# Performance work log

Measured on AMD Instinct MI355X. Metric: run time of the kernel, lower is better.

Reference implementation:

```python
import jax, jax.numpy as jnp
import numpy as np

B, N, D = 2, 2048, 512
H, VD = 8, 64  # v_dim = hid_dim / n_head


def setup_inputs() -> dict:
    key = jax.random.key(0)
    k1, k2, k3, k4 = jax.random.split(key, 4)
    inputs = jax.random.normal(k1, (B, N, D), dtype=jnp.float32)
    # lecun_normal: std = 1/sqrt(fan_in) with fan_in = D
    s = 1.0 / np.sqrt(D)
    q_w = jax.random.normal(k2, (H, D, VD), dtype=jnp.float32) * s
    k_w = jax.random.normal(k3, (H, D, VD), dtype=jnp.float32) * s
    v_w = jax.random.normal(k4, (H, D, VD), dtype=jnp.float32) * s
    return {"inputs": inputs, "q_w": q_w, "k_w": k_w, "v_w": v_w}


def reference(inputs, q_w, k_w, v_w):
    # QKV projections: [B,N,D] x [H,D,VD] -> [B,H,N,VD]
    q = jnp.einsum('bnj,hjk->bhnk', inputs, q_w)
    k = jnp.einsum('bnj,hjk->bhnk', inputs, k_w)
    v = jnp.einsum('bnj,hjk->bhnk', inputs, v_w)
    scale = 1.0 / jnp.sqrt(jnp.asarray(VD, dtype=q.dtype))
    scores = jnp.einsum('bhik,bhjk->bhij', q, k) * scale  # [B,H,N,N]
    att = jax.nn.softmax(scores, axis=-1)
    out = jnp.einsum('bhnj,bhjd->bhnd', att, v)  # [B,H,N,VD]
    out = jnp.transpose(out, (0, 2, 1, 3)).reshape(inputs.shape[0], -1, H * VD)  # [B,N,hid_dim]
    # keras GELU default is exact (non-approximate)
    return jax.nn.gelu(out, approximate=False)
```

## Files before the change

kernel.cpp:

```cpp
#include <hip/hip_runtime.h>
#include <hip/hip_bf16.h>
#include <math.h>

#define BB 2
#define NN 2048
#define DD 512
#define HH 8
#define VD 64

typedef _Float16 half8 __attribute__((ext_vector_type(8)));
typedef _Float16 half4 __attribute__((ext_vector_type(4)));
typedef __fp16 fp16x2 __attribute__((ext_vector_type(2)));
typedef float f32x4 __attribute__((ext_vector_type(4)));

#define GLDS16(gp, lp) __builtin_amdgcn_global_load_lds( \
    (const __attribute__((address_space(1))) void*)(gp), \
    (__attribute__((address_space(3))) void*)(lp), 16, 0, 0)

__device__ __forceinline__ float fexp2(float x) {
#if __has_builtin(__builtin_amdgcn_exp2f)
    return __builtin_amdgcn_exp2f(x);
#else
    return exp2f(x);
#endif
}

__device__ __forceinline__ void stage8(const _Float16* gsrc, size_t ldg, int r0,
                                       _Float16* lbase, int lane) {
    int r8 = lane >> 3;
    int ce = ((lane & 7) ^ r8) << 3;
    const _Float16* g = gsrc + (size_t)(r0 + r8) * ldg + ce;
    GLDS16(g, lbase);
}

__device__ __forceinline__ half8 frag_ld(const _Float16* tile, int row, int cb) {
    int off = row * 128 + (cb ^ ((row & 7) << 4));
    return *(const half8*)((const char*)tile + off);
}

__device__ __forceinline__ half8 frag_ldv(const _Float16* tile, int row, int cb) {
    int off = row * 256 + (cb ^ ((row & 15) << 4));
    return *(const half8*)((const char*)tile + off);
}

__device__ __forceinline__ float gelu_exact(float v) {
    return 0.5f * v * (1.f + erff(v * 0.70710678118654752f));
}

__global__ __launch_bounds__(256) void prep_kernel(
    const float* __restrict__ x,
    const float* __restrict__ qw, const float* __restrict__ kw,
    const float* __restrict__ vw,
    _Float16* __restrict__ wt, _Float16* __restrict__ xh)
{
    __shared__ float ls[64][65];
    const int t = threadIdx.x;
    const int bid = blockIdx.x;
    if (bid < 192) {
        const int kc = bid & 7, h = (bid >> 3) & 7, ty = bid >> 6;
        const float* src = (ty == 0) ? qw : (ty == 1) ? kw : vw;
#pragma unroll
        for (int j = 0; j < 4; ++j) {
            int idx = t + 256 * j;
            int k = idx >> 4, o4 = idx & 15;
            float4 v = *(const float4*)(src + ((size_t)(h * DD + kc * 64 + k) * VD + o4 * 4));
            ls[k][o4 * 4 + 0] = v.x; ls[k][o4 * 4 + 1] = v.y;
            ls[k][o4 * 4 + 2] = v.z; ls[k][o4 * 4 + 3] = v.w;
        }
        __syncthreads();
#pragma unroll
        for (int j = 0; j < 4; ++j) {
            int idx = t + 256 * j;
            int o = idx >> 4, k4 = idx & 15;
            half4 hv;
#pragma unroll
            for (int i = 0; i < 4; ++i) hv[i] = (_Float16)ls[k4 * 4 + i][o];
            *(half4*)(wt + ((size_t)(ty * HH + h) * VD + o) * DD + kc * 64 + k4 * 4) = hv;
        }
    } else {
        size_t idx = ((size_t)(bid - 192) * 256 + t) * 8;
        float4 a = *(const float4*)(x + idx);
        float4 b = *(const float4*)(x + idx + 4);
        half8 hv;
        hv[0] = (_Float16)a.x; hv[1] = (_Float16)a.y;
        hv[2] = (_Float16)a.z; hv[3] = (_Float16)a.w;
        hv[4] = (_Float16)b.x; hv[5] = (_Float16)b.y;
        hv[6] = (_Float16)b.z; hv[7] = (_Float16)b.w;
        *(half8*)(xh + idx) = hv;
    }
}

__global__ __launch_bounds__(256, 1) void qkv_proj_kernel(
    const _Float16* __restrict__ xh,
    const _Float16* __restrict__ wt,
    _Float16* __restrict__ qsp,
    _Float16* __restrict__ kbp,
    _Float16* __restrict__ vtp)
{
    __shared__ __align__(16) _Float16 xls[2][8192];
    __shared__ __align__(16) _Float16 wls[2][12288];
    const int t = threadIdx.x;
    const int wave = t >> 6, lane = t & 63;
    const int lq = lane & 15, g = lane >> 4;
    const int bid = blockIdx.x;
    const int h = bid & 7;
    const int m0 = (bid >> 3) * 128;
    const int rbase = 64 * (wave >> 1);
    const int cbase = 96 * (wave & 1);

    f32x4 acc[4][6];
#pragma unroll
    for (int a = 0; a < 4; ++a)
#pragma unroll
        for (int c = 0; c < 6; ++c) acc[a][c] = (f32x4){0.f, 0.f, 0.f, 0.f};

    auto stage = [&](int buf, int ks) {
#pragma unroll
        for (int j = 0; j < 4; ++j) {
            int i = wave * 4 + j;
            stage8(xh + (size_t)m0 * DD + ks * 64, DD, i * 8, &xls[buf][i * 512], lane);
        }
#pragma unroll
        for (int j = 0; j < 6; ++j) {
            int i = wave * 6 + j;
            int ty = i >> 3;
            int ol = (i & 7) * 8;
            stage8(wt + ((size_t)(ty * HH + h) * VD + ol) * DD + ks * 64, DD, 0,
                   &wls[buf][i * 512], lane);
        }
    };

    stage(0, 0);
    stage(1, 1);
    for (int ks = 0; ks < 8; ++ks) {
        const int buf = ks & 1;
        if (ks < 7) asm volatile("s_waitcnt vmcnt(10)" ::: "memory");
        else        asm volatile("s_waitcnt vmcnt(0)" ::: "memory");
        __builtin_amdgcn_s_barrier();
        half8 af[4][2];
        half8 bf[6][2];
#pragma unroll
        for (int amt = 0; amt < 4; ++amt) {
            af[amt][0] = frag_ld(xls[buf], rbase + amt * 16 + lq, 16 * g);
            af[amt][1] = frag_ld(xls[buf], rbase + amt * 16 + lq, 64 + 16 * g);
        }
#pragma unroll
        for (int ct = 0; ct < 6; ++ct) {
            int wr = cbase + ct * 16 + lq;
            bf[ct][0] = frag_ld(wls[buf], wr, 16 * g);
            bf[ct][1] = frag_ld(wls[buf], wr, 64 + 16 * g);
        }
        asm volatile("s_waitcnt lgkmcnt(0)" ::: "memory");
        __builtin_amdgcn_sched_barrier(0);
        __builtin_amdgcn_s_barrier();
        if (ks + 2 < 8) stage(buf, ks + 2);
        __builtin_amdgcn_s_setprio(1);
#pragma unroll
        for (int ct = 0; ct < 6; ++ct) {
#pragma unroll
            for (int amt = 0; amt < 4; ++amt) {
                acc[amt][ct] = __builtin_amdgcn_mfma_f32_16x16x32_f16(af[amt][0], bf[ct][0], acc[amt][ct], 0, 0, 0);
                acc[amt][ct] = __builtin_amdgcn_mfma_f32_16x16x32_f16(af[amt][1], bf[ct][1], acc[amt][ct], 0, 0, 0);
            }
        }
        __builtin_amdgcn_s_setprio(0);
    }

#pragma unroll
    for (int ct = 0; ct < 6; ++ct) {
        int gcol = cbase + ct * 16 + lq;
        int ty = gcol >> 6, o = gcol & 63;
#pragma unroll
        for (int amt = 0; amt < 4; ++amt) {
#pragma unroll
            for (int i = 0; i < 4; ++i) {
                int ng = m0 + rbase + amt * 16 + 4 * g + i;
                int b = ng >> 11, nb = ng & (NN - 1);
                size_t bh = (size_t)(b * HH + h);
                float v = acc[amt][ct][i];
                if (ty == 0)      qsp[(bh * NN + nb) * VD + o] = (_Float16)(v * 0.18033688011112042f);
                else if (ty == 1) kbp[(bh * NN + nb) * VD + o] = (_Float16)v;
                else {
                    int nbp = (nb & ~31) | (((nb >> 2) & 3) << 3) | (((nb >> 4) & 1) << 2) | (nb & 3);
                    vtp[(bh * VD + o) * NN + nbp] = (_Float16)v;
                }
            }
        }
    }
}

__global__ __launch_bounds__(256, 2) void attn_kernel(
    const _Float16* __restrict__ qs,
    const _Float16* __restrict__ kb,
    const _Float16* __restrict__ vt,
    float* __restrict__ out)
{
    constexpr int NITER = NN / 128;
    __shared__ __align__(16) char SM[65536 + 1024];
    const int t = threadIdx.x;
    const int wave = t >> 6, lane = t & 63;
    const int lq = lane & 15, g = lane >> 4;
    const int bid = blockIdx.x;
    const int xcd = bid & 7;
    const int bh = xcd * 2 + ((bid >> 3) & 1);
    const int qt = bid >> 4;
    const int qbase = qt * 64;

    half8 qf[4][2];
#pragma unroll
    for (int qg = 0; qg < 4; ++qg)
#pragma unroll
        for (int ds = 0; ds < 2; ++ds)
            qf[qg][ds] = *(const half8*)(qs + ((size_t)bh * NN + qbase + 16 * qg + lq) * VD + 32 * ds + 8 * g);

    const int r8 = lane >> 3;
    const _Float16* kS = kb + ((size_t)bh * NN + 32 * wave + r8) * VD + 8 * ((lane & 7) ^ r8);
    const _Float16* vS[4];
#pragma unroll
    for (int uu = 0; uu < 4; ++uu) {
        int vrow = 16 * wave + 4 * uu + g;
        vS[uu] = vt + ((size_t)bh * VD + vrow) * NN + 8 * (lq ^ (vrow & 15));
    }

    _Float16* kb0 = (_Float16*)(SM);
    _Float16* vb0 = (_Float16*)(SM + 16384);
    _Float16* kb1 = (_Float16*)(SM + 32768);
    _Float16* vb1 = (_Float16*)(SM + 49152);

    auto stage = [&](int b, int j) {
        _Float16* kd = (b ? kb1 : kb0) + 4 * wave * 512;
        const _Float16* kp = kS + (size_t)j * 128 * VD;
#pragma unroll
        for (int uu = 0; uu < 4; ++uu)
            GLDS16(kp + uu * 8 * VD, kd + uu * 512);
        _Float16* vd = (b ? vb1 : vb0) + 4 * wave * 512;
#pragma unroll
        for (int uu = 0; uu < 4; ++uu)
            GLDS16(vS[uu] + j * 128, vd + uu * 512);
    };

    f32x4 oacc[4][4];
    f32x4 oacc_l[4];
#pragma unroll
    for (int qg = 0; qg < 4; ++qg) {
#pragma unroll
        for (int dt = 0; dt < 4; ++dt) oacc[qg][dt] = (f32x4){0.f, 0.f, 0.f, 0.f};
        oacc_l[qg] = (f32x4){0.f, 0.f, 0.f, 0.f};
    }
    half8 vones;
#pragma unroll
    for (int i = 0; i < 8; ++i) vones[i] = (_Float16)1.0f;

    stage(0, 0);
    stage(1, 1);

    union PU { fp16x2 h2[4]; half8 h8; };

    for (int j = 0; j < NITER; ++j) {
        const int b = j & 1;
        if (j < NITER - 1) asm volatile("s_waitcnt vmcnt(8)" ::: "memory");
        else               asm volatile("s_waitcnt vmcnt(0)" ::: "memory");
        __builtin_amdgcn_s_barrier();
        const _Float16* kB = b ? kb1 : kb0;
        const _Float16* vB = b ? vb1 : vb0;
        half8 kf[2][2], vf[4];
#pragma unroll
        for (int mt = 0; mt < 2; ++mt)
#pragma unroll
            for (int ds = 0; ds < 2; ++ds)
                kf[mt][ds] = frag_ld(kB, 32 * wave + 16 * mt + lq, 64 * ds + 16 * g);
#pragma unroll
        for (int dt = 0; dt < 4; ++dt)
            vf[dt] = frag_ldv(vB, 16 * dt + lq, 64 * wave + 16 * g);
        asm volatile("s_waitcnt lgkmcnt(0)" ::: "memory");
        __builtin_amdgcn_sched_barrier(0);
        __builtin_amdgcn_s_barrier();
        if (j + 2 < NITER) stage(b, j + 2);
        f32x4 sc[2][2];
        __builtin_amdgcn_s_setprio(1);
#pragma unroll
        for (int mt = 0; mt < 2; ++mt) {
            sc[0][mt] = (f32x4){0.f, 0.f, 0.f, 0.f};
            sc[0][mt] = __builtin_amdgcn_mfma_f32_16x16x32_f16(kf[mt][0], qf[0][0], sc[0][mt], 0, 0, 0);
            sc[0][mt] = __builtin_amdgcn_mfma_f32_16x16x32_f16(kf[mt][1], qf[0][1], sc[0][mt], 0, 0, 0);
        }
#pragma unroll
        for (int qg = 0; qg < 4; ++qg) {
            const int cur = qg & 1;
            if (qg < 3) {
#pragma unroll
                for (int mt = 0; mt < 2; ++mt) {
                    sc[cur ^ 1][mt] = (f32x4){0.f, 0.f, 0.f, 0.f};
                    sc[cur ^ 1][mt] = __builtin_amdgcn_mfma_f32_16x16x32_f16(kf[mt][0], qf[qg + 1][0], sc[cur ^ 1][mt], 0, 0, 0);
                    sc[cur ^ 1][mt] = __builtin_amdgcn_mfma_f32_16x16x32_f16(kf[mt][1], qf[qg + 1][1], sc[cur ^ 1][mt], 0, 0, 0);
                }
            }
            PU pu;
            {
                float p00 = fexp2(sc[cur][0][0]);
                float p01 = fexp2(sc[cur][0][1]);
                float p02 = fexp2(sc[cur][0][2]);
                float p03 = fexp2(sc[cur][0][3]);
                float p10 = fexp2(sc[cur][1][0]);
                float p11 = fexp2(sc[cur][1][1]);
                float p12 = fexp2(sc[cur][1][2]);
                float p13 = fexp2(sc[cur][1][3]);
                pu.h2[0] = __builtin_amdgcn_cvt_pkrtz(p00, p01);
                pu.h2[1] = __builtin_amdgcn_cvt_pkrtz(p02, p03);
                pu.h2[2] = __builtin_amdgcn_cvt_pkrtz(p10, p11);
                pu.h2[3] = __builtin_amdgcn_cvt_pkrtz(p12, p13);
            }
#pragma unroll
            for (int dt = 0; dt < 4; ++dt)
                oacc[qg][dt] = __builtin_amdgcn_mfma_f32_16x16x32_f16(vf[dt], pu.h8, oacc[qg][dt], 0, 0, 0);
            oacc_l[qg] = __builtin_amdgcn_mfma_f32_16x16x32_f16(vones, pu.h8, oacc_l[qg], 0, 0, 0);
        }
        __builtin_amdgcn_s_setprio(0);
    }

    float* lsm  = (float*)(SM + 65536);
    float* sred = (float*)SM;
    __syncthreads();
    if (g == 0) {
#pragma unroll
        for (int qg = 0; qg < 4; ++qg) lsm[wave * 64 + 16 * qg + lq] = oacc_l[qg][0];
    }
#pragma unroll
    for (int qg = 0; qg < 4; ++qg)
#pragma unroll
        for (int dt = 0; dt < 4; ++dt)
            *(f32x4*)(sred + (size_t)wave * 4096 + (16 * qg + lq) * 64 + 16 * dt + 4 * g) = oacc[qg][dt];
    __syncthreads();
    const int b2 = bh >> 3, h = bh & 7;
    const int q = t >> 2, cg = t & 3;
    float lt = (lsm[q] + lsm[64 + q]) + (lsm[128 + q] + lsm[192 + q]);
    float inv = 1.f / lt;
    float* op = out + ((size_t)b2 * NN + qbase + q) * (HH * VD) + h * VD + 16 * cg;
#pragma unroll
    for (int c2 = 0; c2 < 4; ++c2) {
        int off = q * 64 + 16 * cg + 4 * c2;
        f32x4 o = *(const f32x4*)(sred + off);
        o += *(const f32x4*)(sred + 4096 + off);
        o += *(const f32x4*)(sred + 8192 + off);
        o += *(const f32x4*)(sred + 12288 + off);
        float4 r;
        r.x = gelu_exact(o[0] * inv);
        r.y = gelu_exact(o[1] * inv);
        r.z = gelu_exact(o[2] * inv);
        r.w = gelu_exact(o[3] * inv);
        *(float4*)(op + 4 * c2) = r;
    }
}

extern "C" void kernel_launch(void* const* d_in, const int* in_sizes, int n_in,
                              void* d_out, int out_size, void* d_ws, size_t ws_size,
                              hipStream_t stream)
{
    const float* x  = (const float*)d_in[0];
    const float* qw = (const float*)d_in[1];
    const float* kw = (const float*)d_in[2];
    const float* vw = (const float*)d_in[3];
    float* out = (float*)d_out;

    _Float16* wt  = (_Float16*)d_ws;
    _Float16* xhp = wt  + 786432;
    _Float16* qsp = xhp + 2097152;
    _Float16* kbp = qsp + 2097152;
    _Float16* vtp = kbp + 2097152;

    hipLaunchKernelGGL(prep_kernel, dim3(192 + 1024), dim3(256), 0, stream,
                       x, qw, kw, vw, wt, xhp);
    hipLaunchKernelGGL(qkv_proj_kernel, dim3(256), dim3(256), 0, stream,
                       xhp, wt, qsp, kbp, vtp);
    hipLaunchKernelGGL(attn_kernel, dim3(512), dim3(256), 0, stream,
                       qsp, kbp, vtp, out);
}
```

Before: 53.36 us.

## Fuse fp32-to-fp16 input conversion into QKV projection, halve row tile

The prep kernel no longer converts the fp32 input to a half-precision workspace copy. The projection kernel now loads fp32 rows of x straight into registers, converts them, and writes swizzled fp16 into shared memory inside its double-buffered pipeline. The M tile drops from 128 to 64 rows and the launch bound of 1 is removed, so the grid doubles to 512 blocks for better CU coverage. This removes a full write and re-read of the converted input, but it doubles global reads of the weights across the extra blocks and adds register-staged loads whose vmcnt accounting must still hold.

```diff
diff --git a/kernel.cpp b/kernel.cpp
--- a/kernel.cpp
+++ b/kernel.cpp
@@ -48,78 +48,61 @@
 }
 
 __global__ __launch_bounds__(256) void prep_kernel(
-    const float* __restrict__ x,
     const float* __restrict__ qw, const float* __restrict__ kw,
-    const float* __restrict__ vw,
-    _Float16* __restrict__ wt, _Float16* __restrict__ xh)
+    const float* __restrict__ vw, _Float16* __restrict__ wt)
 {
     __shared__ float ls[64][65];
     const int t = threadIdx.x;
     const int bid = blockIdx.x;
-    if (bid < 192) {
-        const int kc = bid & 7, h = (bid >> 3) & 7, ty = bid >> 6;
-        const float* src = (ty == 0) ? qw : (ty == 1) ? kw : vw;
-#pragma unroll
-        for (int j = 0; j < 4; ++j) {
-            int idx = t + 256 * j;
-            int k = idx >> 4, o4 = idx & 15;
-            float4 v = *(const float4*)(src + ((size_t)(h * DD + kc * 64 + k) * VD + o4 * 4));
-            ls[k][o4 * 4 + 0] = v.x; ls[k][o4 * 4 + 1] = v.y;
-            ls[k][o4 * 4 + 2] = v.z; ls[k][o4 * 4 + 3] = v.w;
-        }
-        __syncthreads();
-#pragma unroll
-        for (int j = 0; j < 4; ++j) {
-            int idx = t + 256 * j;
-            int o = idx >> 4, k4 = idx & 15;
-            half4 hv;
-#pragma unroll
-            for (int i = 0; i < 4; ++i) hv[i] = (_Float16)ls[k4 * 4 + i][o];
-            *(half4*)(wt + ((size_t)(ty * HH + h) * VD + o) * DD + kc * 64 + k4 * 4) = hv;
-        }
-    } else {
-        size_t idx = ((size_t)(bid - 192) * 256 + t) * 8;
-        float4 a = *(const float4*)(x + idx);
-        float4 b = *(const float4*)(x + idx + 4);
-        half8 hv;
-        hv[0] = (_Float16)a.x; hv[1] = (_Float16)a.y;
-        hv[2] = (_Float16)a.z; hv[3] = (_Float16)a.w;
-        hv[4] = (_Float16)b.x; hv[5] = (_Float16)b.y;
-        hv[6] = (_Float16)b.z; hv[7] = (_Float16)b.w;
-        *(half8*)(xh + idx) = hv;
-    }
-}
-
-__global__ __launch_bounds__(256, 1) void qkv_proj_kernel(
-    const _Float16* __restrict__ xh,
+    const int kc = bid & 7, h = (bid >> 3) & 7, ty = bid >> 6;
+    const float* src = (ty == 0) ? qw : (ty == 1) ? kw : vw;
+#pragma unroll
+    for (int j = 0; j < 4; ++j) {
+        int idx = t + 256 * j;
+        int k = idx >> 4, o4 = idx & 15;
+        float4 v = *(const float4*)(src + ((size_t)(h * DD + kc * 64 + k) * VD + o4 * 4));
+        ls[k][o4 * 4 + 0] = v.x; ls[k][o4 * 4 + 1] = v.y;
+        ls[k][o4 * 4 + 2] = v.z; ls[k][o4 * 4 + 3] = v.w;
+    }
+    __syncthreads();
+#pragma unroll
+    for (int j = 0; j < 4; ++j) {
+        int idx = t + 256 * j;
+        int o = idx >> 4, k4 = idx & 15;
+        half4 hv;
+#pragma unroll
+        for (int i = 0; i < 4; ++i) hv[i] = (_Float16)ls[k4 * 4 + i][o];
+        *(half4*)(wt + ((size_t)(ty * HH + h) * VD + o) * DD + kc * 64 + k4 * 4) = hv;
+    }
+}
+
+__global__ __launch_bounds__(256) void qkv_proj_kernel(
+    const float* __restrict__ x,
     const _Float16* __restrict__ wt,
     _Float16* __restrict__ qsp,
     _Float16* __restrict__ kbp,
     _Float16* __restrict__ vtp)
 {
-    __shared__ __align__(16) _Float16 xls[2][8192];
+    __shared__ __align__(16) _Float16 xls[2][4096];
     __shared__ __align__(16) _Float16 wls[2][12288];
     const int t = threadIdx.x;
     const int wave = t >> 6, lane = t & 63;
     const int lq = lane & 15, g = lane >> 4;
     const int bid = blockIdx.x;
     const int h = bid & 7;
-    const int m0 = (bid >> 3) * 128;
-    const int rbase = 64 * (wave >> 1);
+    const int m0 = (bid >> 3) * 64;
+    const int rbase = 32 * (wave >> 1);
     const int cbase = 96 * (wave & 1);
-
-    f32x4 acc[4][6];
-#pragma unroll
-    for (int a = 0; a < 4; ++a)
+    const int r8 = lane >> 3;
+    const int ce = ((lane & 7) ^ r8) * 8;
+
+    f32x4 acc[2][6];
+#pragma unroll
+    for (int a = 0; a < 2; ++a)
 #pragma unroll
         for (int c = 0; c < 6; ++c) acc[a][c] = (f32x4){0.f, 0.f, 0.f, 0.f};
 
-    auto stage = [&](int buf, int ks) {
-#pragma unroll
-        for (int j = 0; j < 4; ++j) {
-            int i = wave * 4 + j;
-            stage8(xh + (size_t)m0 * DD + ks * 64, DD, i * 8, &xls[buf][i * 512], lane);
-        }
+    auto stage_w = [&](int buf, int ks) {
 #pragma unroll
         for (int j = 0; j < 6; ++j) {
             int i = wave * 6 + j;
@@ -130,48 +113,68 @@
         }
     };
 
-    stage(0, 0);
-    stage(1, 1);
-    for (int ks = 0; ks < 8; ++ks) {
-        const int buf = ks & 1;
-        if (ks < 7) asm volatile("s_waitcnt vmcnt(10)" ::: "memory");
-        else        asm volatile("s_waitcnt vmcnt(0)" ::: "memory");
-        __builtin_amdgcn_s_barrier();
-        half8 af[4][2];
-        half8 bf[6][2];
-#pragma unroll
-        for (int amt = 0; amt < 4; ++amt) {
-            af[amt][0] = frag_ld(xls[buf], rbase + amt * 16 + lq, 16 * g);
-            af[amt][1] = frag_ld(xls[buf], rbase + amt * 16 + lq, 64 + 16 * g);
-        }
-#pragma unroll
-        for (int ct = 0; ct < 6; ++ct) {
-            int wr = cbase + ct * 16 + lq;
-            bf[ct][0] = frag_ld(wls[buf], wr, 16 * g);
-            bf[ct][1] = frag_ld(wls[buf], wr, 64 + 16 * g);
-        }
-        asm volatile("s_waitcnt lgkmcnt(0)" ::: "memory");
-        __builtin_amdgcn_sched_barrier(0);
-        __builtin_amdgcn_s_barrier();
-        if (ks + 2 < 8) stage(buf, ks + 2);
-        __builtin_amdgcn_s_setprio(1);
-#pragma unroll
-        for (int ct = 0; ct < 6; ++ct) {
-#pragma unroll
-            for (int amt = 0; amt < 4; ++amt) {
-                acc[amt][ct] = __builtin_amdgcn_mfma_f32_16x16x32_f16(af[amt][0], bf[ct][0], acc[amt][ct], 0, 0, 0);
-                acc[amt][ct] = __builtin_amdgcn_mfma_f32_16x16x32_f16(af[amt][1], bf[ct][1], acc[amt][ct], 0, 0, 0);
-            }
-        }
-        __builtin_amdgcn_s_setprio(0);
-    }
+    float4 xrA[4], xrB[4];
+#define PJ_LOADX(XR, KS)                                                         \
+    _Pragma("unroll") for (int jj = 0; jj < 2; ++jj) {                           \
+        const float* xp = x + (size_t)(m0 + (wave * 2 + jj) * 8 + r8) * DD + (KS) * 64 + ce; \
+        XR[2 * jj]     = *(const float4*)xp;                                     \
+        XR[2 * jj + 1] = *(const float4*)(xp + 4);                               \
+    }
+
+    PJ_LOADX(xrA, 0); stage_w(0, 0);
+    PJ_LOADX(xrB, 1); stage_w(1, 1);
+
+#define PJ_ITER(KS, BUF, XR)                                                     \
+    {                                                                            \
+        if ((KS) < 7) asm volatile("s_waitcnt vmcnt(10)" ::: "memory");          \
+        else          asm volatile("s_waitcnt vmcnt(0)" ::: "memory");           \
+        _Pragma("unroll") for (int jj = 0; jj < 2; ++jj) {                       \
+            half8 hv;                                                            \
+            hv[0] = (_Float16)XR[2 * jj].x;     hv[1] = (_Float16)XR[2 * jj].y;  \
+            hv[2] = (_Float16)XR[2 * jj].z;     hv[3] = (_Float16)XR[2 * jj].w;  \
+            hv[4] = (_Float16)XR[2 * jj + 1].x; hv[5] = (_Float16)XR[2 * jj + 1].y; \
+            hv[6] = (_Float16)XR[2 * jj + 1].z; hv[7] = (_Float16)XR[2 * jj + 1].w; \
+            *(half8*)&xls[BUF][(wave * 2 + jj) * 512 + lane * 8] = hv;           \
+        }                                                                        \
+        asm volatile("s_waitcnt lgkmcnt(0)" ::: "memory");                       \
+        __builtin_amdgcn_s_barrier();                                            \
+        half8 af[2][2];                                                          \
+        half8 bf[6][2];                                                          \
+        _Pragma("unroll") for (int amt = 0; amt < 2; ++amt) {                    \
+            af[amt][0] = frag_ld(xls[BUF], rbase + amt * 16 + lq, 16 * g);       \
+            af[amt][1] = frag_ld(xls[BUF], rbase + amt * 16 + lq, 64 + 16 * g);  \
+        }                                                                        \
+        _Pragma("unroll") for (int ct = 0; ct < 6; ++ct) {                       \
+            int wr = cbase + ct * 16 + lq;                                       \
+            bf[ct][0] = frag_ld(wls[BUF], wr, 16 * g);                           \
+            bf[ct][1] = frag_ld(wls[BUF], wr, 64 + 16 * g);                      \
+        }                                                                        \
+        asm volatile("s_waitcnt lgkmcnt(0)" ::: "memory");                       \
+        __builtin_amdgcn_sched_barrier(0);                                       \
+        __builtin_amdgcn_s_barrier();                                            \
+        if ((KS) + 2 < 8) { PJ_LOADX(XR, (KS) + 2); stage_w(BUF, (KS) + 2); }    \
+        __builtin_amdgcn_s_setprio(1);                                           \
+        _Pragma("unroll") for (int ct = 0; ct < 6; ++ct)                         \
+            _Pragma("unroll") for (int amt = 0; amt < 2; ++amt) {                \
+                acc[amt][ct] = __builtin_amdgcn_mfma_f32_16x16x32_f16(af[amt][0], bf[ct][0], acc[amt][ct], 0, 0, 0); \
+                acc[amt][ct] = __builtin_amdgcn_mfma_f32_16x16x32_f16(af[amt][1], bf[ct][1], acc[amt][ct], 0, 0, 0); \
+            }                                                                    \
+        __builtin_amdgcn_s_setprio(0);                                           \
+    }
+
+    for (int ks2 = 0; ks2 < 8; ks2 += 2) {
+        PJ_ITER(ks2, 0, xrA);
+        PJ_ITER(ks2 + 1, 1, xrB);
+    }
+#undef PJ_ITER
+#undef PJ_LOADX
 
 #pragma unroll
     for (int ct = 0; ct < 6; ++ct) {
         int gcol = cbase + ct * 16 + lq;
         int ty = gcol >> 6, o = gcol & 63;
 #pragma unroll
-        for (int amt = 0; amt < 4; ++amt) {
+        for (int amt = 0; amt < 2; ++amt) {
 #pragma unroll
             for (int i = 0; i < 4; ++i) {
                 int ng = m0 + rbase + amt * 16 + 4 * g + i;
@@ -363,15 +366,14 @@
     float* out = (float*)d_out;
 
     _Float16* wt  = (_Float16*)d_ws;
-    _Float16* xhp = wt  + 786432;
-    _Float16* qsp = xhp + 2097152;
+    _Float16* qsp = wt  + 786432;
     _Float16* kbp = qsp + 2097152;
     _Float16* vtp = kbp + 2097152;
 
-    hipLaunchKernelGGL(prep_kernel, dim3(192 + 1024), dim3(256), 0, stream,
-                       x, qw, kw, vw, wt, xhp);
-    hipLaunchKernelGGL(qkv_proj_kernel, dim3(256), dim3(256), 0, stream,
-                       xhp, wt, qsp, kbp, vtp);
+    hipLaunchKernelGGL(prep_kernel, dim3(192), dim3(256), 0, stream,
+                       qw, kw, vw, wt);
+    hipLaunchKernelGGL(qkv_proj_kernel, dim3(512), dim3(256), 0, stream,
+                       x, wt, qsp, kbp, vtp);
     hipLaunchKernelGGL(attn_kernel, dim3(512), dim3(256), 0, stream,
                        qsp, kbp, vtp, out);
 }
```

Result: slower. 54.75 us (+2.6%).
